# Optimization experiments

Hardware: AMD Instinct MI355X
Metric: run time of the kernel (lower is better)

## Reference

```python
import jax, jax.numpy as jnp
import numpy as np

N_NODES = 10000
N_EDGES = 640000
CH = 128


def setup_inputs() -> dict:
    key = jax.random.key(0)
    ks = jax.random.split(key, 12)
    inp = {
        "node_feat": jax.random.normal(ks[0], (N_NODES, 118), dtype=jnp.float32),
        "edge_feat": jax.random.normal(ks[1], (N_EDGES, 22), dtype=jnp.float32),
        "src": jax.random.randint(ks[2], (N_EDGES,), 0, N_NODES),
        "dst": jax.random.randint(ks[3], (N_EDGES,), 0, N_NODES),
        "W_node": jax.random.normal(ks[4], (118, CH), dtype=jnp.float32) * 0.05,
        "b_node": jax.random.normal(ks[5], (CH,), dtype=jnp.float32) * 0.05,
        "W_edge": jax.random.normal(ks[6], (22, CH), dtype=jnp.float32) * 0.05,
        "b_edge": jax.random.normal(ks[7], (CH,), dtype=jnp.float32) * 0.05,
        "W_a1": jax.random.normal(ks[8], (2 * CH, CH), dtype=jnp.float32) * 0.05,
        "b_a1": jax.random.normal(ks[9], (CH,), dtype=jnp.float32) * 0.05,
        "W_a2": jax.random.normal(ks[10], (CH, 1), dtype=jnp.float32) * 0.05,
        "b_a2": jax.random.normal(ks[11], (1,), dtype=jnp.float32) * 0.05,
        "layer_num": 3,
    }
    return inp


def reference(node_feat, edge_feat, src, dst, W_node, b_node, W_edge, b_edge,
              W_a1, b_a1, W_a2, b_a2, layer_num):
    # node_map / edge_map (apply_nodes / apply_edges)
    h = node_feat @ W_node + b_node          # [N, C] node hidden
    eh = edge_feat @ W_edge + b_edge         # [E, C] edge hidden (stored on graph, unused by attn)
    e = None
    for _ in range(layer_num):
        # per-edge gather of src/dst hidden, concat -> small 2-layer MLP
        cat = jnp.concatenate([h[src], h[dst]], axis=-1)   # [E, 2C]
        x = jax.nn.leaky_relu(cat @ W_a1 + b_a1)           # torch default slope 0.01
        e = x @ W_a2 + b_a2                                # [E, 1]
    return e
```

## Files before the change

kernel.cpp:

```cpp
#include <hip/hip_runtime.h>
#include <hip/hip_bf16.h>

#define N_NODES 10000
#define N_EDGES 640000
#define CH 128
#define KN 118

typedef _Float16 h2 __attribute__((ext_vector_type(2)));
typedef _Float16 h8 __attribute__((ext_vector_type(8)));

#define H2_OF(v, k) __builtin_shufflevector((v), (v), 2 * (k), 2 * (k) + 1)

__global__ __launch_bounds__(128) void k1_weights(
    const float* __restrict__ Wn, const float* __restrict__ bn,
    const float* __restrict__ Wa1, const float* __restrict__ ba1,
    const float* __restrict__ w2, float* __restrict__ M,
    float* __restrict__ V, _Float16* __restrict__ w2h) {
  int c = threadIdx.x;
  int mat = blockIdx.x / 119;
  int i = blockIdx.x % 119;
  if (mat == 2) {
    w2h[c] = (_Float16)w2[c];
    return;
  }
  const float* B = Wa1 + mat * CH * CH;
  const float* a = (i < KN) ? (Wn + i * CH) : bn;
  float acc = 0.f;
#pragma unroll 8
  for (int j = 0; j < CH; ++j) acc = fmaf(a[j], B[j * CH + c], acc);
  if (i < KN) {
    M[(mat * KN + i) * CH + c] = acc;
  } else {
    if (mat == 1) acc += ba1[c];
    V[mat * CH + c] = acc;
  }
}

__global__ __launch_bounds__(256) void k2_nodes(
    const float* __restrict__ nf, const float* __restrict__ M,
    const float* __restrict__ V, _Float16* __restrict__ T) {
  int tx = threadIdx.x;
  int c = tx & (CH - 1);
  int mat = tx >> 7;
  int n0 = blockIdx.x * 16;
  const float* Mm = M + mat * KN * CH + c;
  const float* r = nf + (size_t)n0 * KN;
  float acc[16];
#pragma unroll
  for (int j = 0; j < 16; ++j) acc[j] = 0.f;
#pragma unroll 2
  for (int k = 0; k < KN; ++k) {
    float m = Mm[k * CH];
#pragma unroll
    for (int j = 0; j < 16; ++j) acc[j] = fmaf(r[j * KN + k], m, acc[j]);
  }
  float v = V[mat * CH + c];
  _Float16* t = T + (size_t)mat * N_NODES * CH + c;
#pragma unroll
  for (int j = 0; j < 16; ++j)
    t[(size_t)(n0 + j) * CH] = (_Float16)(acc[j] + v);
}

__device__ inline float edge_acc8(h8 s, h8 d, h8 w) {
  h8 t = s + d;
  h8 p = t * (_Float16)0.01f;
  h8 u = __builtin_elementwise_max(t, p);
  float acc = 0.f;
  acc = __builtin_amdgcn_fdot2(H2_OF(u, 0), H2_OF(w, 0), acc, false);
  acc = __builtin_amdgcn_fdot2(H2_OF(u, 1), H2_OF(w, 1), acc, false);
  acc = __builtin_amdgcn_fdot2(H2_OF(u, 2), H2_OF(w, 2), acc, false);
  acc = __builtin_amdgcn_fdot2(H2_OF(u, 3), H2_OF(w, 3), acc, false);
  return acc;
}

__global__ __launch_bounds__(256) void k3_edges(
    const int* __restrict__ src, const int* __restrict__ dst,
    const _Float16* __restrict__ S, const _Float16* __restrict__ D,
    const _Float16* __restrict__ w2h, const float* __restrict__ b2,
    float* __restrict__ out) {
  int tid = blockIdx.x * 256 + threadIdx.x;
  int g = tid >> 4;
  int sub = tid & 15;
  int c0 = sub << 3;

  h8 w = *(const h8*)(w2h + c0);
  int4 s4 = *(const int4*)(src + 4 * g);
  int4 d4 = *(const int4*)(dst + 4 * g);

  const _Float16* Sp = S + c0;
  const _Float16* Dp = D + c0;
  h8 sr0 = *(const h8*)(Sp + ((size_t)s4.x << 7));
  h8 dr0 = *(const h8*)(Dp + ((size_t)d4.x << 7));
  h8 sr1 = *(const h8*)(Sp + ((size_t)s4.y << 7));
  h8 dr1 = *(const h8*)(Dp + ((size_t)d4.y << 7));
  h8 sr2 = *(const h8*)(Sp + ((size_t)s4.z << 7));
  h8 dr2 = *(const h8*)(Dp + ((size_t)d4.z << 7));
  h8 sr3 = *(const h8*)(Sp + ((size_t)s4.w << 7));
  h8 dr3 = *(const h8*)(Dp + ((size_t)d4.w << 7));

  float a0 = edge_acc8(sr0, dr0, w);
  float a1 = edge_acc8(sr1, dr1, w);
  float a2 = edge_acc8(sr2, dr2, w);
  float a3 = edge_acc8(sr3, dr3, w);

  float r0 = a0 + __shfl_xor(a0, 1);
  float r1 = a1 + __shfl_xor(a1, 1);
  float r2 = a2 + __shfl_xor(a2, 1);
  float r3 = a3 + __shfl_xor(a3, 1);
  float v1 = (sub & 1) ? r1 : r0;
  float v2 = (sub & 1) ? r3 : r2;
  float t1 = v1 + __shfl_xor(v1, 2);
  float t2 = v2 + __shfl_xor(v2, 2);
  float u = (sub & 2) ? t2 : t1;
  u += __shfl_xor(u, 4);
  u += __shfl_xor(u, 8);

  if (sub < 4) out[4 * g + sub] = u + b2[0];
}

extern "C" void kernel_launch(void* const* d_in, const int* in_sizes, int n_in,
                              void* d_out, int out_size, void* d_ws, size_t ws_size,
                              hipStream_t stream) {
  const float* nf  = (const float*)d_in[0];
  const int*   src = (const int*)d_in[2];
  const int*   dst = (const int*)d_in[3];
  const float* Wn  = (const float*)d_in[4];
  const float* bn  = (const float*)d_in[5];
  const float* Wa1 = (const float*)d_in[8];
  const float* ba1 = (const float*)d_in[9];
  const float* Wa2 = (const float*)d_in[10];
  const float* ba2 = (const float*)d_in[11];
  float* out = (float*)d_out;

  char* ws = (char*)d_ws;
  float* M = (float*)ws;
  float* V = (float*)(ws + 2 * KN * CH * sizeof(float));
  _Float16* w2h = (_Float16*)(ws + (2 * KN * CH + 2 * CH) * sizeof(float));
  _Float16* T = (_Float16*)((char*)w2h + CH * sizeof(_Float16));
  _Float16* S = T;
  _Float16* D = T + (size_t)N_NODES * CH;

  k1_weights<<<239, 128, 0, stream>>>(Wn, bn, Wa1, ba1, Wa2, M, V, w2h);
  k2_nodes<<<N_NODES / 16, 256, 0, stream>>>(nf, M, V, T);
  k3_edges<<<(N_EDGES / 4 * 16) / 256, 256, 0, stream>>>(src, dst, S, D, w2h, ba2, out);
}
```

Before: 166.9 us.

## Compute node projection with MFMA using transposed fp16 weights in swizzled LDS

The folded node-to-attention weight matrix is now stored transposed in fp16 and zero-padded to 128 along K. The node GEMM is rewritten to use 16x16x32 fp16 MFMA instructions, with B staged in XOR-swizzled shared memory and A loaded per lane from the fp32 node features. This replaces the scalar FMA loop in the node kernel. It adds fp16 rounding of the weights and inputs, and a 64KB LDS load in every block, which limits occupancy.

```diff
diff --git a/kernel.cpp b/kernel.cpp
--- a/kernel.cpp
+++ b/kernel.cpp
@@ -8,19 +8,24 @@
 
 typedef _Float16 h2 __attribute__((ext_vector_type(2)));
 typedef _Float16 h8 __attribute__((ext_vector_type(8)));
+typedef float f32x4 __attribute__((ext_vector_type(4)));
 
 #define H2_OF(v, k) __builtin_shufflevector((v), (v), 2 * (k), 2 * (k) + 1)
 
 __global__ __launch_bounds__(128) void k1_weights(
     const float* __restrict__ Wn, const float* __restrict__ bn,
     const float* __restrict__ Wa1, const float* __restrict__ ba1,
-    const float* __restrict__ w2, float* __restrict__ M,
+    const float* __restrict__ w2, _Float16* __restrict__ Mt,
     float* __restrict__ V, _Float16* __restrict__ w2h) {
   int c = threadIdx.x;
   int mat = blockIdx.x / 119;
   int i = blockIdx.x % 119;
   if (mat == 2) {
     w2h[c] = (_Float16)w2[c];
+#pragma unroll
+    for (int cg = c; cg < 256; cg += 128)
+#pragma unroll
+      for (int p = 118; p < 128; ++p) Mt[cg * 128 + p] = (_Float16)0.f;
     return;
   }
   const float* B = Wa1 + mat * CH * CH;
@@ -28,37 +33,76 @@
   float acc = 0.f;
 #pragma unroll 8
   for (int j = 0; j < CH; ++j) acc = fmaf(a[j], B[j * CH + c], acc);
+  int cg = mat * CH + c;
   if (i < KN) {
-    M[(mat * KN + i) * CH + c] = acc;
+    Mt[cg * 128 + i] = (_Float16)acc;
   } else {
     if (mat == 1) acc += ba1[c];
-    V[mat * CH + c] = acc;
+    V[cg] = acc;
   }
 }
 
-__global__ __launch_bounds__(256) void k2_nodes(
-    const float* __restrict__ nf, const float* __restrict__ M,
+__global__ __launch_bounds__(128) void k2_mfma(
+    const float* __restrict__ nf, const _Float16* __restrict__ Mt,
     const float* __restrict__ V, _Float16* __restrict__ T) {
+  __shared__ _Float16 Blds[256 * 128];
   int tx = threadIdx.x;
-  int c = tx & (CH - 1);
-  int mat = tx >> 7;
-  int n0 = blockIdx.x * 16;
-  const float* Mm = M + mat * KN * CH + c;
-  const float* r = nf + (size_t)n0 * KN;
-  float acc[16];
+
 #pragma unroll
-  for (int j = 0; j < 16; ++j) acc[j] = 0.f;
-#pragma unroll 2
-  for (int k = 0; k < KN; ++k) {
-    float m = Mm[k * CH];
+  for (int it = 0; it < 32; ++it) {
+    int chunk = it * 128 + tx;
+    int cg = chunk >> 4;
+    int k0 = (chunk & 15) << 3;
+    h8 v = *(const h8*)(Mt + cg * 128 + k0);
+    *(h8*)(Blds + cg * 128 + (k0 ^ ((cg & 7) << 3))) = v;
+  }
+
+  int wave = tx >> 6;
+  int lane = tx & 63;
+  int m = lane & 15;
+  int quad = lane >> 4;
+  int nbase = blockIdx.x * 32 + wave * 16;
+  int node = nbase + m;
+  const float* arow = nf + (size_t)(node < N_NODES ? node : 0) * KN;
+
+  h8 afrag[4];
 #pragma unroll
-    for (int j = 0; j < 16; ++j) acc[j] = fmaf(r[j * KN + k], m, acc[j]);
+  for (int s = 0; s < 4; ++s) {
+#pragma unroll
+    for (int j = 0; j < 8; ++j) {
+      int k = s * 32 + quad * 8 + j;
+      afrag[s][j] = (k < KN) ? (_Float16)arow[k] : (_Float16)0.f;
+    }
   }
-  float v = V[mat * CH + c];
-  _Float16* t = T + (size_t)mat * N_NODES * CH + c;
+  __syncthreads();
+
+  f32x4 acc[16];
 #pragma unroll
-  for (int j = 0; j < 16; ++j)
-    t[(size_t)(n0 + j) * CH] = (_Float16)(acc[j] + v);
+  for (int ct = 0; ct < 16; ++ct) acc[ct] = f32x4{0.f, 0.f, 0.f, 0.f};
+  int swz = (m & 7) << 3;
+#pragma unroll
+  for (int ct = 0; ct < 16; ++ct) {
+    const _Float16* brow = Blds + (ct * 16 + m) * 128;
+#pragma unroll
+    for (int s = 0; s < 4; ++s) {
+      h8 b = *(const h8*)(brow + ((s * 32 + quad * 8) ^ swz));
+      acc[ct] = __builtin_amdgcn_mfma_f32_16x16x32_f16(afrag[s], b, acc[ct], 0, 0, 0);
+    }
+  }
+
+#pragma unroll
+  for (int ct = 0; ct < 16; ++ct) {
+    int cg = ct * 16 + m;
+    float bias = V[cg];
+    int mat = cg >> 7;
+    int cc = cg & (CH - 1);
+    int nd0 = nbase + quad * 4;
+    _Float16* tp = T + ((size_t)mat * N_NODES + nd0) * CH + cc;
+#pragma unroll
+    for (int r = 0; r < 4; ++r) {
+      if (nd0 + r < N_NODES) tp[(size_t)r * CH] = (_Float16)(acc[ct][r] + bias);
+    }
+  }
 }
 
 __device__ inline float edge_acc8(h8 s, h8 d, h8 w) {
@@ -133,14 +177,14 @@
   float* out = (float*)d_out;
 
   char* ws = (char*)d_ws;
-  float* M = (float*)ws;
-  float* V = (float*)(ws + 2 * KN * CH * sizeof(float));
-  _Float16* w2h = (_Float16*)(ws + (2 * KN * CH + 2 * CH) * sizeof(float));
-  _Float16* T = (_Float16*)((char*)w2h + CH * sizeof(_Float16));
+  _Float16* Mt  = (_Float16*)ws;
+  float*    V   = (float*)(ws + 256 * 128 * sizeof(_Float16));
+  _Float16* w2h = (_Float16*)((char*)V + 256 * sizeof(float));
+  _Float16* T   = (_Float16*)((char*)w2h + 128 * sizeof(_Float16));
   _Float16* S = T;
   _Float16* D = T + (size_t)N_NODES * CH;
 
-  k1_weights<<<239, 128, 0, stream>>>(Wn, bn, Wa1, ba1, Wa2, M, V, w2h);
-  k2_nodes<<<N_NODES / 16, 256, 0, stream>>>(nf, M, V, T);
+  k1_weights<<<239, 128, 0, stream>>>(Wn, bn, Wa1, ba1, Wa2, Mt, V, w2h);
+  k2_mfma<<<(N_NODES + 31) / 32, 128, 0, stream>>>(nf, Mt, V, T);
   k3_edges<<<(N_EDGES / 4 * 16) / 256, 256, 0, stream>>>(src, dst, S, D, w2h, ba2, out);
 }
```

New measurement: 145.8 us. 12.6% less time.
